# Kernel tuning notes

Hardware: AMD Instinct MI355X
Metric: run time of the kernel (lower is better)

The kernel has to match this reference:

```python
import jax, jax.numpy as jnp
import numpy as np

P = 1048576      # number of sampled ray points
H = 524288       # number of sparse voxels
NEMB = 600000    # number of corner embeddings (total_num_embedding)
D = 32           # voxel_embed_dim
VOXEL_SIZE = 0.25


def setup_inputs() -> dict:
    key = jax.random.key(0)
    k1, k2, k3, k4, k5 = jax.random.split(key, 5)
    point_xyz = jax.random.normal(k1, (H, 3), dtype=jnp.float32) * 5.0
    values = jax.random.normal(k2, (NEMB, D), dtype=jnp.float32)
    sampled_idx = jax.random.randint(k3, (P,), 0, H, dtype=jnp.int64)
    point_feats = jax.random.randint(k4, (H, 8), 0, NEMB, dtype=jnp.int64)
    # sample points lie inside their voxel (realistic, keeps interp weights in [0,1])
    jitter = (jax.random.uniform(k5, (P, 3), dtype=jnp.float32) - 0.5) * VOXEL_SIZE
    sampled_xyz = point_xyz[sampled_idx] + jitter
    return {
        "sampled_xyz": sampled_xyz,
        "point_xyz": point_xyz,
        "values": values,
        "sampled_idx": sampled_idx,
        "point_feats": point_feats,
    }


def _corner_q(dtype):
    # offset_points(p, 0.5, offset_only=True) + 0.5 -> {0,1}^3 corners, torch 'ij' meshgrid order
    c = jnp.arange(2)
    q = jnp.stack(jnp.meshgrid(c, c, c, indexing="ij"), axis=-1).reshape(8, 3)
    return q.astype(dtype)  # [8,3]


def reference(sampled_xyz, point_xyz, values, sampled_idx, point_feats):
    # gather per-sample voxel center and its 8 corner embedding ids
    pxyz = point_xyz[sampled_idx]        # [P,3]
    pf = point_feats[sampled_idx]        # [P,8]
    feats = values[pf]                   # [P,8,D]  (F.embedding)
    # normalized position inside voxel, in [0,1]^3
    p = (sampled_xyz - pxyz) / VOXEL_SIZE + 0.5   # [P,3]
    q = _corner_q(p.dtype)                        # [8,3]
    # trilinear weights: prod over xyz of (p*q + (1-p)*(1-q))
    w = jnp.prod(p[:, None, :] * q[None] + (1.0 - p[:, None, :]) * (1.0 - q[None]), axis=-1)  # [P,8]
    return jnp.einsum("pc,pcd->pd", w, feats)     # [P,D]
```

## Files before the change

kernel.cpp:

```cpp
#include <hip/hip_runtime.h>


#define VOXEL_INV 4.0f
#define CAP 8

typedef float vfloat4 __attribute__((ext_vector_type(4)));

__device__ __forceinline__ void corner_ids(const int* __restrict__ point_feats,
                                           int vi, int* ids)
{
    const int4* pf4 = (const int4*)(point_feats + ((size_t)vi << 3));
    int4 f0 = pf4[0];
    int4 f1 = pf4[1];
    ids[0] = f0.x; ids[1] = f0.y; ids[2] = f0.z; ids[3] = f0.w;
    ids[4] = f1.x; ids[5] = f1.y; ids[6] = f1.z; ids[7] = f1.w;
}

__device__ void compute_point_direct(
    const float* __restrict__ point_xyz,
    const float* __restrict__ values,
    const int*   __restrict__ point_feats,
    float*       __restrict__ out,
    int vi, int p, float sx, float sy, float sz)
{
    float cx = point_xyz[(size_t)vi * 3 + 0];
    float cy = point_xyz[(size_t)vi * 3 + 1];
    float cz = point_xyz[(size_t)vi * 3 + 2];

    float px = (sx - cx) * VOXEL_INV + 0.5f;
    float py = (sy - cy) * VOXEL_INV + 0.5f;
    float pz = (sz - cz) * VOXEL_INV + 0.5f;

    float xs[2] = {1.0f - px, px};
    float ys[2] = {1.0f - py, py};
    float zs[2] = {1.0f - pz, pz};

    int ids[8];
    corner_ids(point_feats, vi, ids);

    vfloat4 acc[8] = {};
#pragma unroll
    for (int c = 0; c < 8; ++c) {
        float w = xs[(c >> 2) & 1] * ys[(c >> 1) & 1] * zs[c & 1];
        const vfloat4* vr = (const vfloat4*)(values + ((size_t)ids[c] << 5));
#pragma unroll
        for (int k = 0; k < 8; ++k) acc[k] += w * vr[k];
    }
    vfloat4* o = (vfloat4*)(out + ((size_t)p << 5));
#pragma unroll
    for (int k = 0; k < 8; ++k) __builtin_nontemporal_store(acc[k], o + k);
}

__global__ __launch_bounds__(256) void svenc_direct(
    const float* __restrict__ sampled_xyz,
    const float* __restrict__ point_xyz,
    const float* __restrict__ values,
    const int*   __restrict__ sampled_idx,
    const int*   __restrict__ point_feats,
    float*       __restrict__ out,
    int P)
{
    int t   = blockIdx.x * blockDim.x + threadIdx.x;
    int pid = t >> 3;
    int sub = t & 7;
    if (pid >= P) return;

    int vi = __builtin_nontemporal_load(sampled_idx + pid);
    float sx = __builtin_nontemporal_load(sampled_xyz + pid * 3 + 0);
    float sy = __builtin_nontemporal_load(sampled_xyz + pid * 3 + 1);
    float sz = __builtin_nontemporal_load(sampled_xyz + pid * 3 + 2);

    float cx = point_xyz[(size_t)vi * 3 + 0];
    float cy = point_xyz[(size_t)vi * 3 + 1];
    float cz = point_xyz[(size_t)vi * 3 + 2];

    float px = (sx - cx) * VOXEL_INV + 0.5f;
    float py = (sy - cy) * VOXEL_INV + 0.5f;
    float pz = (sz - cz) * VOXEL_INV + 0.5f;

    float xs[2] = {1.0f - px, px};
    float ys[2] = {1.0f - py, py};
    float zs[2] = {1.0f - pz, pz};

    int ids[8];
    corner_ids(point_feats, vi, ids);

    vfloat4 acc = {0.0f, 0.0f, 0.0f, 0.0f};
#pragma unroll
    for (int c = 0; c < 8; ++c) {
        float w = xs[(c >> 2) & 1] * ys[(c >> 1) & 1] * zs[c & 1];
        const vfloat4 v = ((const vfloat4*)(values + ((size_t)ids[c] << 5)))[sub];
        acc += w * v;
    }
    __builtin_nontemporal_store(acc, (vfloat4*)(out + ((size_t)pid << 5)) + sub);
}

__global__ __launch_bounds__(256) void k_bucket_xyz(
    const float* __restrict__ sampled_xyz,
    const float* __restrict__ point_xyz,
    const float* __restrict__ values,
    const int*   __restrict__ sampled_idx,
    const int*   __restrict__ point_feats,
    float*       __restrict__ out,
    int*         __restrict__ counts,
    vfloat4*     __restrict__ bucket,
    int P)
{
    int p = blockIdx.x * 256 + threadIdx.x;
    if (p >= P) return;

    int vi = __builtin_nontemporal_load(sampled_idx + p);

    int pos = atomicAdd(counts + vi, 1);

    float sx = __builtin_nontemporal_load(sampled_xyz + (size_t)p * 3 + 0);
    float sy = __builtin_nontemporal_load(sampled_xyz + (size_t)p * 3 + 1);
    float sz = __builtin_nontemporal_load(sampled_xyz + (size_t)p * 3 + 2);

    if (pos < CAP) {
        vfloat4 e;
        e.x = __int_as_float(p);
        e.y = sx; e.z = sy; e.w = sz;
        __builtin_nontemporal_store(e, bucket + ((size_t)vi << 3) + pos);
    } else {
        compute_point_direct(point_xyz, values, point_feats, out, vi, p, sx, sy, sz);
    }
}

__global__ __launch_bounds__(256) void svenc_voxel_xyz(
    const float* __restrict__ point_xyz,
    const float* __restrict__ values,
    const int*   __restrict__ point_feats,
    const int*   __restrict__ counts,
    const vfloat4* __restrict__ bucket,
    float*       __restrict__ out,
    int H)
{
    int t   = blockIdx.x * 256 + threadIdx.x;
    int g   = t >> 3;
    int sub = t & 7;
    if (g >= H) return;

    int n = __builtin_nontemporal_load(counts + g);
    if (n == 0) return;
    if (n > CAP) n = CAP;

    float cx = point_xyz[(size_t)g * 3 + 0];
    float cy = point_xyz[(size_t)g * 3 + 1];
    float cz = point_xyz[(size_t)g * 3 + 2];

    int ids[8];
    corner_ids(point_feats, g, ids);

    vfloat4 v[8];
#pragma unroll
    for (int c = 0; c < 8; ++c)
        v[c] = ((const vfloat4*)(values + ((size_t)ids[c] << 5)))[sub];

    for (int i = 0; i < n; ++i) {
        vfloat4 e = __builtin_nontemporal_load(bucket + ((size_t)g << 3) + i);
        int p = __float_as_int(e.x);

        float px = (e.y - cx) * VOXEL_INV + 0.5f;
        float py = (e.z - cy) * VOXEL_INV + 0.5f;
        float pz = (e.w - cz) * VOXEL_INV + 0.5f;

        float xs[2] = {1.0f - px, px};
        float ys[2] = {1.0f - py, py};
        float zs[2] = {1.0f - pz, pz};

        vfloat4 acc = {0.0f, 0.0f, 0.0f, 0.0f};
#pragma unroll
        for (int c = 0; c < 8; ++c) {
            float w = xs[(c >> 2) & 1] * ys[(c >> 1) & 1] * zs[c & 1];
            acc += w * v[c];
        }
        __builtin_nontemporal_store(acc, (vfloat4*)(out + ((size_t)p << 5)) + sub);
    }
}

__global__ __launch_bounds__(256) void k_bucket_id(
    const float* __restrict__ sampled_xyz,
    const float* __restrict__ point_xyz,
    const float* __restrict__ values,
    const int*   __restrict__ sampled_idx,
    const int*   __restrict__ point_feats,
    float*       __restrict__ out,
    int*         __restrict__ counts,
    int*         __restrict__ bucket,
    int P)
{
    int p = blockIdx.x * 256 + threadIdx.x;
    if (p >= P) return;

    int vi = sampled_idx[p];
    int pos = atomicAdd(counts + vi, 1);
    if (pos < CAP) {
        __builtin_nontemporal_store(p, bucket + ((size_t)vi << 3) + pos);
    } else {
        float sx = sampled_xyz[(size_t)p * 3 + 0];
        float sy = sampled_xyz[(size_t)p * 3 + 1];
        float sz = sampled_xyz[(size_t)p * 3 + 2];
        compute_point_direct(point_xyz, values, point_feats, out, vi, p, sx, sy, sz);
    }
}

__global__ __launch_bounds__(256) void svenc_voxel_id(
    const float* __restrict__ sampled_xyz,
    const float* __restrict__ point_xyz,
    const float* __restrict__ values,
    const int*   __restrict__ point_feats,
    const int*   __restrict__ counts,
    const int*   __restrict__ bucket,
    float*       __restrict__ out,
    int H)
{
    int t   = blockIdx.x * 256 + threadIdx.x;
    int g   = t >> 3;
    int sub = t & 7;
    if (g >= H) return;

    int n = counts[g];
    if (n == 0) return;
    if (n > CAP) n = CAP;

    float cx = point_xyz[(size_t)g * 3 + 0];
    float cy = point_xyz[(size_t)g * 3 + 1];
    float cz = point_xyz[(size_t)g * 3 + 2];

    int ids[8];
    corner_ids(point_feats, g, ids);

    vfloat4 v[8];
#pragma unroll
    for (int c = 0; c < 8; ++c)
        v[c] = ((const vfloat4*)(values + ((size_t)ids[c] << 5)))[sub];

    for (int i = 0; i < n; ++i) {
        int p = bucket[((size_t)g << 3) + i];

        float sx = sampled_xyz[(size_t)p * 3 + 0];
        float sy = sampled_xyz[(size_t)p * 3 + 1];
        float sz = sampled_xyz[(size_t)p * 3 + 2];

        float px = (sx - cx) * VOXEL_INV + 0.5f;
        float py = (sy - cy) * VOXEL_INV + 0.5f;
        float pz = (sz - cz) * VOXEL_INV + 0.5f;

        float xs[2] = {1.0f - px, px};
        float ys[2] = {1.0f - py, py};
        float zs[2] = {1.0f - pz, pz};

        vfloat4 acc = {0.0f, 0.0f, 0.0f, 0.0f};
#pragma unroll
        for (int c = 0; c < 8; ++c) {
            float w = xs[(c >> 2) & 1] * ys[(c >> 1) & 1] * zs[c & 1];
            acc += w * v[c];
        }
        __builtin_nontemporal_store(acc, (vfloat4*)(out + ((size_t)p << 5)) + sub);
    }
}

extern "C" void kernel_launch(void* const* d_in, const int* in_sizes, int n_in,
                              void* d_out, int out_size, void* d_ws, size_t ws_size,
                              hipStream_t stream) {
    const float* sampled_xyz = (const float*)d_in[0];
    const float* point_xyz   = (const float*)d_in[1];
    const float* values      = (const float*)d_in[2];
    const int*   sampled_idx = (const int*)d_in[3];
    const int*   point_feats = (const int*)d_in[4];
    float* out = (float*)d_out;

    int P = in_sizes[3];

    int H;
    if (in_sizes[0] == 3 * P)       H = in_sizes[4] / 8;
    else                            H = in_sizes[4];

    size_t bucketB_xyz = (size_t)H * CAP * 16;
    size_t need_xyz    = bucketB_xyz + (size_t)H * 4;
    size_t bucketB_id  = (size_t)H * CAP * 4;
    size_t need_id     = bucketB_id + (size_t)H * 4;

    int gp = (P + 255) / 256;
    long tt = (long)H * 8;
    int gm = (int)((tt + 255) / 256);

    if (d_ws != nullptr && ws_size >= need_xyz && H > 0) {
        vfloat4* bucket = (vfloat4*)d_ws;
        int* counts = (int*)((char*)d_ws + bucketB_xyz);
        hipMemsetAsync(counts, 0, (size_t)H * 4, stream);
        k_bucket_xyz<<<gp, 256, 0, stream>>>(
            sampled_xyz, point_xyz, values, sampled_idx, point_feats,
            out, counts, bucket, P);
        svenc_voxel_xyz<<<gm, 256, 0, stream>>>(
            point_xyz, values, point_feats, counts, bucket, out, H);
    } else if (d_ws != nullptr && ws_size >= need_id && H > 0) {
        int* bucket = (int*)d_ws;
        int* counts = (int*)((char*)d_ws + bucketB_id);
        hipMemsetAsync(counts, 0, (size_t)H * 4, stream);
        k_bucket_id<<<gp, 256, 0, stream>>>(
            sampled_xyz, point_xyz, values, sampled_idx, point_feats,
            out, counts, bucket, P);
        svenc_voxel_id<<<gm, 256, 0, stream>>>(
            sampled_xyz, point_xyz, values, point_feats, counts, bucket, out, H);
    } else {
        long total_threads = (long)P * 8;
        int grid = (int)((total_threads + 255) / 256);
        svenc_direct<<<grid, 256, 0, stream>>>(
            sampled_xyz, point_xyz, values, sampled_idx, point_feats, out, P);
    }
}
```

Baseline: 362.3 us.

## Drop xyz-packed bucket path; use id buckets with shuffle-broadcast slot loads

Removes the 16-byte-per-entry bucket path that stored point index plus xyz, so the id-only bucket path (4 bytes per entry) now always runs. In the per-voxel kernel each of the 8 lanes loads one bucket slot, and the point indices are broadcast with a wavefront shuffle instead of every lane reloading each slot. The aim is to cut bucket write and read traffic. The cost is that sampled_xyz must now be gathered at random positions in the second pass, and the bucket store becomes a normal cached store.

```diff
diff --git a/kernel.cpp b/kernel.cpp
--- a/kernel.cpp
+++ b/kernel.cpp
@@ -95,90 +95,6 @@
     __builtin_nontemporal_store(acc, (vfloat4*)(out + ((size_t)pid << 5)) + sub);
 }
 
-__global__ __launch_bounds__(256) void k_bucket_xyz(
-    const float* __restrict__ sampled_xyz,
-    const float* __restrict__ point_xyz,
-    const float* __restrict__ values,
-    const int*   __restrict__ sampled_idx,
-    const int*   __restrict__ point_feats,
-    float*       __restrict__ out,
-    int*         __restrict__ counts,
-    vfloat4*     __restrict__ bucket,
-    int P)
-{
-    int p = blockIdx.x * 256 + threadIdx.x;
-    if (p >= P) return;
-
-    int vi = __builtin_nontemporal_load(sampled_idx + p);
-
-    int pos = atomicAdd(counts + vi, 1);
-
-    float sx = __builtin_nontemporal_load(sampled_xyz + (size_t)p * 3 + 0);
-    float sy = __builtin_nontemporal_load(sampled_xyz + (size_t)p * 3 + 1);
-    float sz = __builtin_nontemporal_load(sampled_xyz + (size_t)p * 3 + 2);
-
-    if (pos < CAP) {
-        vfloat4 e;
-        e.x = __int_as_float(p);
-        e.y = sx; e.z = sy; e.w = sz;
-        __builtin_nontemporal_store(e, bucket + ((size_t)vi << 3) + pos);
-    } else {
-        compute_point_direct(point_xyz, values, point_feats, out, vi, p, sx, sy, sz);
-    }
-}
-
-__global__ __launch_bounds__(256) void svenc_voxel_xyz(
-    const float* __restrict__ point_xyz,
-    const float* __restrict__ values,
-    const int*   __restrict__ point_feats,
-    const int*   __restrict__ counts,
-    const vfloat4* __restrict__ bucket,
-    float*       __restrict__ out,
-    int H)
-{
-    int t   = blockIdx.x * 256 + threadIdx.x;
-    int g   = t >> 3;
-    int sub = t & 7;
-    if (g >= H) return;
-
-    int n = __builtin_nontemporal_load(counts + g);
-    if (n == 0) return;
-    if (n > CAP) n = CAP;
-
-    float cx = point_xyz[(size_t)g * 3 + 0];
-    float cy = point_xyz[(size_t)g * 3 + 1];
-    float cz = point_xyz[(size_t)g * 3 + 2];
-
-    int ids[8];
-    corner_ids(point_feats, g, ids);
-
-    vfloat4 v[8];
-#pragma unroll
-    for (int c = 0; c < 8; ++c)
-        v[c] = ((const vfloat4*)(values + ((size_t)ids[c] << 5)))[sub];
-
-    for (int i = 0; i < n; ++i) {
-        vfloat4 e = __builtin_nontemporal_load(bucket + ((size_t)g << 3) + i);
-        int p = __float_as_int(e.x);
-
-        float px = (e.y - cx) * VOXEL_INV + 0.5f;
-        float py = (e.z - cy) * VOXEL_INV + 0.5f;
-        float pz = (e.w - cz) * VOXEL_INV + 0.5f;
-
-        float xs[2] = {1.0f - px, px};
-        float ys[2] = {1.0f - py, py};
-        float zs[2] = {1.0f - pz, pz};
-
-        vfloat4 acc = {0.0f, 0.0f, 0.0f, 0.0f};
-#pragma unroll
-        for (int c = 0; c < 8; ++c) {
-            float w = xs[(c >> 2) & 1] * ys[(c >> 1) & 1] * zs[c & 1];
-            acc += w * v[c];
-        }
-        __builtin_nontemporal_store(acc, (vfloat4*)(out + ((size_t)p << 5)) + sub);
-    }
-}
-
 __global__ __launch_bounds__(256) void k_bucket_id(
     const float* __restrict__ sampled_xyz,
     const float* __restrict__ point_xyz,
@@ -193,10 +109,10 @@
     int p = blockIdx.x * 256 + threadIdx.x;
     if (p >= P) return;
 
-    int vi = sampled_idx[p];
+    int vi = __builtin_nontemporal_load(sampled_idx + p);
     int pos = atomicAdd(counts + vi, 1);
     if (pos < CAP) {
-        __builtin_nontemporal_store(p, bucket + ((size_t)vi << 3) + pos);
+        bucket[((size_t)vi << 3) + pos] = p;
     } else {
         float sx = sampled_xyz[(size_t)p * 3 + 0];
         float sy = sampled_xyz[(size_t)p * 3 + 1];
@@ -218,9 +134,13 @@
     int t   = blockIdx.x * 256 + threadIdx.x;
     int g   = t >> 3;
     int sub = t & 7;
+    int lane = threadIdx.x & 63;
     if (g >= H) return;
 
     int n = counts[g];
+
+    int myslot = bucket[((size_t)g << 3) + sub];
+
     if (n == 0) return;
     if (n > CAP) n = CAP;
 
@@ -236,8 +156,9 @@
     for (int c = 0; c < 8; ++c)
         v[c] = ((const vfloat4*)(values + ((size_t)ids[c] << 5)))[sub];
 
+    int grpbase = lane & 56;
     for (int i = 0; i < n; ++i) {
-        int p = bucket[((size_t)g << 3) + i];
+        int p = __shfl(myslot, grpbase + i, 64);
 
         float sx = sampled_xyz[(size_t)p * 3 + 0];
         float sy = sampled_xyz[(size_t)p * 3 + 1];
@@ -277,31 +198,21 @@
     if (in_sizes[0] == 3 * P)       H = in_sizes[4] / 8;
     else                            H = in_sizes[4];
 
-    size_t bucketB_xyz = (size_t)H * CAP * 16;
-    size_t need_xyz    = bucketB_xyz + (size_t)H * 4;
-    size_t bucketB_id  = (size_t)H * CAP * 4;
-    size_t need_id     = bucketB_id + (size_t)H * 4;
-
-    int gp = (P + 255) / 256;
-    long tt = (long)H * 8;
-    int gm = (int)((tt + 255) / 256);
-
-    if (d_ws != nullptr && ws_size >= need_xyz && H > 0) {
-        vfloat4* bucket = (vfloat4*)d_ws;
-        int* counts = (int*)((char*)d_ws + bucketB_xyz);
+    size_t bucketB = (size_t)H * CAP * 4;
+    size_t need    = bucketB + (size_t)H * 4;
+
+    if (d_ws != nullptr && ws_size >= need && H > 0) {
+        int* bucket = (int*)d_ws;
+        int* counts = (int*)((char*)d_ws + bucketB);
         hipMemsetAsync(counts, 0, (size_t)H * 4, stream);
-        k_bucket_xyz<<<gp, 256, 0, stream>>>(
-            sampled_xyz, point_xyz, values, sampled_idx, point_feats,
-            out, counts, bucket, P);
-        svenc_voxel_xyz<<<gm, 256, 0, stream>>>(
-            point_xyz, values, point_feats, counts, bucket, out, H);
-    } else if (d_ws != nullptr && ws_size >= need_id && H > 0) {
-        int* bucket = (int*)d_ws;
-        int* counts = (int*)((char*)d_ws + bucketB_id);
-        hipMemsetAsync(counts, 0, (size_t)H * 4, stream);
+
+        int gp = (P + 255) / 256;
         k_bucket_id<<<gp, 256, 0, stream>>>(
             sampled_xyz, point_xyz, values, sampled_idx, point_feats,
             out, counts, bucket, P);
+
+        long tt = (long)H * 8;
+        int gm = (int)((tt + 255) / 256);
         svenc_voxel_id<<<gm, 256, 0, stream>>>(
             sampled_xyz, point_xyz, values, point_feats, counts, bucket, out, H);
     } else {
```

Result: slower. 372.1 us (+2.7%).
